# Kernel tuning notes

Measured on AMD Instinct MI355X. Metric: run time of the kernel, lower is better.

The kernel has to match this reference:

```python
import jax, jax.numpy as jnp
import numpy as np

B, N, F, O = 8, 4096, 512, 512
D = F // 8  # fc1/fc2 projection dim = 64


def setup_inputs() -> dict:
    key = jax.random.key(0)
    ks = jax.random.split(key, 8)
    x = jax.random.normal(ks[0], (B, N, F), dtype=jnp.float32)
    mask = jax.random.randint(ks[1], (B, N), 0, 2).astype(jnp.float32)
    s1 = 1.0 / np.sqrt(F)
    w1 = jax.random.uniform(ks[2], (F, D), jnp.float32, -s1, s1)
    b1 = jnp.zeros((D,), jnp.float32)
    w2 = jax.random.uniform(ks[3], (F, D), jnp.float32, -s1, s1)
    b2 = jnp.zeros((D,), jnp.float32)
    s2 = 1.0 / np.sqrt(O)
    weight = jax.random.uniform(ks[4], (F, O), jnp.float32, -s2, s2)
    return {"x": x, "mask": mask, "w1": w1, "b1": b1, "w2": w2, "b2": b2, "weight": weight}


def reference(x, mask, w1, b1, w2, b2, weight):
    # q, k: [B, N, D]
    q = x @ w1 + b1
    k = x @ w2 + b2
    scale = jnp.sqrt(jnp.asarray(D, x.dtype))
    # sim: [B, N, N]
    sim = jnp.einsum('bnd,bmd->bnm', q, k) / scale
    # NOTE: mask.unsqueeze(-1) -> [B, N, 1]: masks QUERY rows (faithful to source)
    neg = jnp.asarray(-1e12, x.dtype)
    sim = sim + (1.0 - mask)[:, :, None] * neg
    adj = jax.nn.softmax(sim, axis=-1) * mask[:, :, None]
    support = x @ weight  # [B, N, O]
    return jnp.einsum('bnm,bmo->bno', adj, support)
```

## Files before the change

kernel.cpp:

```cpp
#include <hip/hip_runtime.h>

constexpr int BB = 8, NN = 4096, FF = 512, DD = 64, OO = 512;

using short8  = __attribute__((ext_vector_type(8))) short;
using ushort8 = __attribute__((ext_vector_type(8))) unsigned short;
using ushort4v= __attribute__((ext_vector_type(4))) unsigned short;
using f32x4   = __attribute__((ext_vector_type(4))) float;

__device__ __forceinline__ unsigned short f2bf(float f) {
  unsigned int u = __builtin_bit_cast(unsigned int, f);
  return (unsigned short)((u + 0x7FFFu + ((u >> 16) & 1u)) >> 16);
}

__device__ __forceinline__ f32x4 mfma16(short8 a, short8 b, f32x4 c) {
  return __builtin_amdgcn_mfma_f32_16x16x32_bf16(a, b, c, 0, 0, 0);
}

__device__ __forceinline__ void gl_lds16(const void* g, void* s) {
  __builtin_amdgcn_global_load_lds(
      (const __attribute__((address_space(1))) unsigned int*)g,
      (__attribute__((address_space(3))) unsigned int*)s,
      16, 0, 0);
}

__global__ void cast_x(const float* __restrict__ x, unsigned short* __restrict__ xb) {
  size_t base = ((size_t)blockIdx.x * 256 + threadIdx.x) * 8;
  float4 a = *(const float4*)(x + base);
  float4 b = *(const float4*)(x + base + 4);
  ushort8 o;
  o[0]=f2bf(a.x); o[1]=f2bf(a.y); o[2]=f2bf(a.z); o[3]=f2bf(a.w);
  o[4]=f2bf(b.x); o[5]=f2bf(b.y); o[6]=f2bf(b.z); o[7]=f2bf(b.w);
  *(ushort8*)(xb + base) = o;
}

__global__ void build_w(const float* __restrict__ w1, const float* __restrict__ w2,
                        const float* __restrict__ wgt,
                        const float* __restrict__ b1, const float* __restrict__ b2,
                        unsigned short* __restrict__ Wt, float* __restrict__ bias) {
  int idx = blockIdx.x * 256 + threadIdx.x;
  int j = idx >> 9, kk = idx & 511;
  float v = (j < 64) ? w1[kk * 64 + j]
          : (j < 128) ? w2[kk * 64 + (j - 64)]
                      : wgt[(size_t)kk * 512 + (j - 128)];
  Wt[(size_t)j * 512 + kk] = f2bf(v);
  if (kk == 0) bias[j] = (j < 64) ? b1[j] : (j < 128) ? b2[j - 64] : 0.f;
}

__global__ void compact_rows(const float* __restrict__ mask, int* __restrict__ cnt,
                             int* __restrict__ ridx) {
  __shared__ int wsum[4];
  __shared__ int base;
  const int b = blockIdx.x;
  const int t = threadIdx.x, lane = t & 63, w = t >> 6;
  if (t == 0) base = 0;
  __syncthreads();
  for (int it = 0; it < 16; ++it) {
    int r = it * 256 + t;
    bool act = mask[(b << 12) + r] != 0.f;
    unsigned long long bal = __ballot(act);
    int pre = __popcll(bal & ((1ull << lane) - 1ull));
    if (lane == 0) wsum[w] = __popcll(bal);
    __syncthreads();
    int woff = 0;
    for (int i = 0; i < w; ++i) woff += wsum[i];
    int tot = wsum[0] + wsum[1] + wsum[2] + wsum[3];
    if (act) ridx[(b << 12) + base + woff + pre] = r;
    __syncthreads();
    if (t == 0) base += tot;
    __syncthreads();
  }
  if (t == 0) cnt[b] = base;
}

__global__ void zero_masked(const float* __restrict__ mask, float* __restrict__ out) {
  int gid = blockIdx.x * 256 + threadIdx.x;
  int r = gid >> 7, c = (gid & 127) * 4;
  if (mask[r] == 0.f) {
    float4 z = {0.f, 0.f, 0.f, 0.f};
    *(float4*)(out + (size_t)r * 512 + c) = z;
  }
}

__global__ __launch_bounds__(256, 2) void proj_gemm(
    const unsigned short* __restrict__ X, const unsigned short* __restrict__ Wt,
    const float* __restrict__ bias,
    unsigned short* __restrict__ QK, unsigned short* __restrict__ SupT) {
  __shared__ __align__(16) unsigned short Abuf[128 * 64];
  __shared__ __align__(16) unsigned short Bbuf[128 * 64];
  const int t = threadIdx.x, lane = t & 63, w = t >> 6;
  const int nblk = blockIdx.x;
  const int m0 = blockIdx.y * 128, n0 = nblk * 128;
  const int wm = w & 1, wn = w >> 1;

  f32x4 acc[4][4] = {};
  for (int kt = 0; kt < 8; ++kt) {
    for (int i = 0; i < 4; ++i) {
      int c = i * 4 + w;
      int row = c * 8 + (lane >> 3);
      int k0 = (lane & 7) * 8;
      gl_lds16(X + (size_t)(m0 + row) * 512 + kt * 64 + k0, &Abuf[c * 512]);
      gl_lds16(Wt + (size_t)(n0 + row) * 512 + kt * 64 + k0, &Bbuf[c * 512]);
    }
    __syncthreads();
    short8 af[4][2], bfr[4][2];
    for (int mi = 0; mi < 4; ++mi)
      for (int kc = 0; kc < 2; ++kc) {
        int row = wm * 64 + mi * 16 + (lane & 15);
        int d = kc * 32 + (lane >> 4) * 8;
        af[mi][kc] = *(const short8*)&Abuf[row * 64 + d];
      }
    for (int ni = 0; ni < 4; ++ni)
      for (int kc = 0; kc < 2; ++kc) {
        int col = wn * 64 + ni * 16 + (lane & 15);
        int d = kc * 32 + (lane >> 4) * 8;
        bfr[ni][kc] = *(const short8*)&Bbuf[col * 64 + d];
      }
    for (int mi = 0; mi < 4; ++mi)
      for (int ni = 0; ni < 4; ++ni)
        for (int kc = 0; kc < 2; ++kc)
          acc[mi][ni] = mfma16(af[mi][kc], bfr[ni][kc], acc[mi][ni]);
    __syncthreads();
  }
  for (int mi = 0; mi < 4; ++mi)
    for (int ni = 0; ni < 4; ++ni) {
      int col_g = n0 + wn * 64 + ni * 16 + (lane & 15);
      int row0 = m0 + wm * 64 + mi * 16 + ((lane >> 4) * 4);
      float bv = bias[col_g];
      if (nblk == 0) {
        for (int j = 0; j < 4; ++j)
          QK[(size_t)(row0 + j) * 128 + col_g] = f2bf(acc[mi][ni][j] + bv);
      } else {
        int scol = col_g - 128;
        int b = row0 >> 12, rl = row0 & 4095;
        ushort4v pk;
        for (int j = 0; j < 4; ++j) pk[j] = f2bf(acc[mi][ni][j] + bv);
        *(ushort4v*)&SupT[(size_t)(b * 512 + scol) * 4096 + rl] = pk;
      }
    }
}

__global__ __launch_bounds__(512, 2) void attn_kernel(
    const unsigned short* __restrict__ QK, const unsigned short* __restrict__ SupT,
    const int* __restrict__ cnt, const int* __restrict__ ridx,
    float* __restrict__ out) {
  __shared__ __align__(16) unsigned short Kb[3][32 * 64];
  __shared__ __align__(16) unsigned short Vt[3][256 * 32];
  __shared__ __align__(16) unsigned short Pb[2][64 * 40];
  __shared__ float lsh[2][64];
  __shared__ int rsh[64];

  const int batch = blockIdx.x & 7;
  const int rest  = blockIdx.x >> 3;
  const int chunk = rest >> 1, colh = rest & 1;
  const int n_act = cnt[batch];
  if (chunk * 64 >= n_act) return;
  const int rem = min(64, n_act - chunk * 64);

  const int t = threadIdx.x, lane = t & 63, w = t >> 6;
  const int keybase = batch << 12;
  const int wm = w >> 2;
  const int wq = w & 3;
  const int fms = wq >> 1, ks = wq & 1;
  const int wo = w & 3;

  if (t < 64) rsh[t] = ridx[(batch << 12) + chunk * 64 + min(t, rem - 1)];
  __syncthreads();

  short8 aq[2];
  {
    int rl = rsh[wm * 32 + fms * 16 + (lane & 15)];
    for (int kc = 0; kc < 2; ++kc)
      aq[kc] = *(const short8*)&QK[(size_t)(keybase + rl) * 128 + kc * 32 + (lane >> 4) * 8];
  }

  f32x4 acc[2][4] = {};
  float lacc[4] = {0.f, 0.f, 0.f, 0.f};

  auto stage = [&](int p, int key0) {
    if (w < 4) {
      int key = w * 8 + (lane >> 3);
      int q = lane & 7;
      int d0 = (q ^ (key & 7)) * 8;
      gl_lds16(QK + (size_t)(keybase + key0 + key) * 128 + 64 + d0, &Kb[p][w * 512]);
    }
    for (int i = 0; i < 2; ++i) {
      int c = i * 8 + w;
      int colL = c * 16 + (lane >> 2);
      int q = lane & 3;
      int k0 = (q ^ ((colL >> 1) & 3)) * 8;
      gl_lds16(SupT + (size_t)(batch * 512 + colh * 256 + colL) * 4096 + key0 + k0,
               &Vt[p][c * 512]);
    }
  };

  stage(0, 0);
  stage(1, 32);
  for (int kt = 0; kt < 128; ++kt) {
    const int p = kt % 3;
    const int pb = kt & 1;
    if (kt < 127) {
      if (w < 4) asm volatile("s_waitcnt vmcnt(3)" ::: "memory");
      else       asm volatile("s_waitcnt vmcnt(2)" ::: "memory");
    } else {
      asm volatile("s_waitcnt vmcnt(0)" ::: "memory");
    }
    asm volatile("s_barrier" ::: "memory");

    if (kt < 126) stage((kt + 2) % 3, (kt + 2) * 32);

    {
      f32x4 sa = {0.f, 0.f, 0.f, 0.f};
      int key = ks * 16 + (lane & 15);
      __builtin_amdgcn_s_setprio(1);
      for (int kc = 0; kc < 2; ++kc) {
        int dblk = kc * 4 + (lane >> 4);
        int blk = dblk ^ (key & 7);
        short8 bk = *(const short8*)&Kb[p][key * 64 + blk * 8];
        sa = mfma16(aq[kc], bk, sa);
      }
      __builtin_amdgcn_s_setprio(0);
      int rl0 = wm * 32 + fms * 16 + (lane >> 4) * 4;
      for (int j = 0; j < 4; ++j) {
        float pv = __expf(sa[j] * 0.125f);
        lacc[j] += pv;
        Pb[pb][(rl0 + j) * 40 + key] = f2bf(pv);
      }
    }
    asm volatile("s_waitcnt lgkmcnt(0)" ::: "memory");
    asm volatile("s_barrier" ::: "memory");

    short8 pa[2];
    for (int fm = 0; fm < 2; ++fm) {
      int row = wm * 32 + fm * 16 + (lane & 15);
      pa[fm] = *(const short8*)&Pb[pb][row * 40 + (lane >> 4) * 8];
    }
    __builtin_amdgcn_s_setprio(1);
    for (int ni = 0; ni < 4; ++ni) {
      int colL = wo * 64 + ni * 16 + (lane & 15);
      int blk = (lane >> 4) ^ ((colL >> 1) & 3);
      short8 vb = *(const short8*)&Vt[p][colL * 32 + blk * 8];
      acc[0][ni] = mfma16(pa[0], vb, acc[0][ni]);
      acc[1][ni] = mfma16(pa[1], vb, acc[1][ni]);
    }
    __builtin_amdgcn_s_setprio(0);
  }

  for (int j = 0; j < 4; ++j) {
    float v = lacc[j];
    v += __shfl_xor(v, 1); v += __shfl_xor(v, 2);
    v += __shfl_xor(v, 4); v += __shfl_xor(v, 8);
    lacc[j] = v;
  }
  if ((lane & 15) == 0) {
    int rl0 = wm * 32 + fms * 16 + (lane >> 4) * 4;
    for (int j = 0; j < 4; ++j) lsh[ks][rl0 + j] = lacc[j];
  }
  __syncthreads();

  for (int fm = 0; fm < 2; ++fm)
    for (int ni = 0; ni < 4; ++ni) {
      int colL = wo * 64 + ni * 16 + (lane & 15);
      int sl0 = wm * 32 + fm * 16 + (lane >> 4) * 4;
      for (int j = 0; j < 4; ++j) {
        if (sl0 + j < rem) {
          float linv = 1.f / (lsh[0][sl0 + j] + lsh[1][sl0 + j]);
          int rl = rsh[sl0 + j];
          out[(size_t)(keybase + rl) * 512 + colh * 256 + colL] = acc[fm][ni][j] * linv;
        }
      }
    }
}

extern "C" void kernel_launch(void* const* d_in, const int* in_sizes, int n_in,
                              void* d_out, int out_size, void* d_ws, size_t ws_size,
                              hipStream_t stream) {
  const float* x    = (const float*)d_in[0];
  const float* mask = (const float*)d_in[1];
  const float* w1   = (const float*)d_in[2];
  const float* b1   = (const float*)d_in[3];
  const float* w2   = (const float*)d_in[4];
  const float* b2   = (const float*)d_in[5];
  const float* wgt  = (const float*)d_in[6];
  float* out = (float*)d_out;

  char* ws = (char*)d_ws;
  unsigned short* Xb   = (unsigned short*)(ws);
  unsigned short* QK   = (unsigned short*)(ws + 33554432);
  unsigned short* SupT = (unsigned short*)(ws + 41943040);
  unsigned short* Wt   = (unsigned short*)(ws + 75497472);
  float* bias          = (float*)(ws + 76152832);
  int*   cnt           = (int*)(ws + 76417536);
  int*   ridx          = (int*)(ws + 76417664);

  build_w<<<dim3(1280), dim3(256), 0, stream>>>(w1, w2, wgt, b1, b2, Wt, bias);
  compact_rows<<<dim3(8), dim3(256), 0, stream>>>(mask, cnt, ridx);
  cast_x<<<dim3(8192), dim3(256), 0, stream>>>(x, Xb);
  proj_gemm<<<dim3(5, 256), dim3(256), 0, stream>>>(Xb, Wt, bias, QK, SupT);
  attn_kernel<<<dim3(1024), dim3(512), 0, stream>>>(QK, SupT, cnt, ridx, out);
  zero_masked<<<dim3(16384), dim3(256), 0, stream>>>(mask, out);
}
```

Baseline: 279.7 us.

## Load K and V fragments directly from global into registers, drop LDS staging

The attention kernel no longer stages K and V tiles through a triple-buffered LDS ring filled by global_load_lds. Each wave now loads its own MFMA operand fragments straight from global memory into registers and prefetches the next tile one iteration ahead, removing the per-tile vmcnt wait and one barrier. Occupancy is raised to 4 blocks per CU because the LDS footprint shrinks. The trade is that K fragments are read redundantly across waves, and V fragments are read redundantly across the two wm wave groups, using global and L2 bandwidth in place of LDS sharing, with only one tile of load latency hidden.

```diff
diff --git a/kernel.cpp b/kernel.cpp
--- a/kernel.cpp
+++ b/kernel.cpp
@@ -139,12 +139,10 @@
     }
 }
 
-__global__ __launch_bounds__(512, 2) void attn_kernel(
+__global__ __launch_bounds__(512, 4) void attn_kernel(
     const unsigned short* __restrict__ QK, const unsigned short* __restrict__ SupT,
     const int* __restrict__ cnt, const int* __restrict__ ridx,
     float* __restrict__ out) {
-  __shared__ __align__(16) unsigned short Kb[3][32 * 64];
-  __shared__ __align__(16) unsigned short Vt[3][256 * 32];
   __shared__ __align__(16) unsigned short Pb[2][64 * 40];
   __shared__ float lsh[2][64];
   __shared__ int rsh[64];
@@ -173,76 +171,68 @@
       aq[kc] = *(const short8*)&QK[(size_t)(keybase + rl) * 128 + kc * 32 + (lane >> 4) * 8];
   }
 
+  const unsigned short* Kp =
+      QK + (size_t)(keybase + ks * 16 + (lane & 15)) * 128 + 64 + (lane >> 4) * 8;
+  const unsigned short* Vp =
+      SupT + (size_t)(batch * 512 + colh * 256 + wo * 64 + (lane & 15)) * 4096 + (lane >> 4) * 8;
+
   f32x4 acc[2][4] = {};
   float lacc[4] = {0.f, 0.f, 0.f, 0.f};
 
-  auto stage = [&](int p, int key0) {
-    if (w < 4) {
-      int key = w * 8 + (lane >> 3);
-      int q = lane & 7;
-      int d0 = (q ^ (key & 7)) * 8;
-      gl_lds16(QK + (size_t)(keybase + key0 + key) * 128 + 64 + d0, &Kb[p][w * 512]);
-    }
-    for (int i = 0; i < 2; ++i) {
-      int c = i * 8 + w;
-      int colL = c * 16 + (lane >> 2);
-      int q = lane & 3;
-      int k0 = (q ^ ((colL >> 1) & 3)) * 8;
-      gl_lds16(SupT + (size_t)(batch * 512 + colh * 256 + colL) * 4096 + key0 + k0,
-               &Vt[p][c * 512]);
-    }
-  };
-
-  stage(0, 0);
-  stage(1, 32);
+  short8 kf0 = *(const short8*)(Kp);
+  short8 kf1 = *(const short8*)(Kp + 32);
+  short8 vf0 = *(const short8*)(Vp);
+  short8 vf1 = *(const short8*)(Vp + (size_t)16 * 4096);
+  short8 vf2 = *(const short8*)(Vp + (size_t)32 * 4096);
+  short8 vf3 = *(const short8*)(Vp + (size_t)48 * 4096);
+
+  const int rl0 = wm * 32 + fms * 16 + (lane >> 4) * 4;
+  const int key = ks * 16 + (lane & 15);
+  const int prow = wm * 32 + (lane & 15);
+  const int pcol = (lane >> 4) * 8;
+
   for (int kt = 0; kt < 128; ++kt) {
-    const int p = kt % 3;
     const int pb = kt & 1;
-    if (kt < 127) {
-      if (w < 4) asm volatile("s_waitcnt vmcnt(3)" ::: "memory");
-      else       asm volatile("s_waitcnt vmcnt(2)" ::: "memory");
-    } else {
-      asm volatile("s_waitcnt vmcnt(0)" ::: "memory");
-    }
-    asm volatile("s_barrier" ::: "memory");
-
-    if (kt < 126) stage((kt + 2) % 3, (kt + 2) * 32);
+    f32x4 sa = {0.f, 0.f, 0.f, 0.f};
+    __builtin_amdgcn_s_setprio(1);
+    sa = mfma16(aq[0], kf0, sa);
+    sa = mfma16(aq[1], kf1, sa);
+    __builtin_amdgcn_s_setprio(0);
 
     {
-      f32x4 sa = {0.f, 0.f, 0.f, 0.f};
-      int key = ks * 16 + (lane & 15);
-      __builtin_amdgcn_s_setprio(1);
-      for (int kc = 0; kc < 2; ++kc) {
-        int dblk = kc * 4 + (lane >> 4);
-        int blk = dblk ^ (key & 7);
-        short8 bk = *(const short8*)&Kb[p][key * 64 + blk * 8];
-        sa = mfma16(aq[kc], bk, sa);
-      }
-      __builtin_amdgcn_s_setprio(0);
-      int rl0 = wm * 32 + fms * 16 + (lane >> 4) * 4;
-      for (int j = 0; j < 4; ++j) {
-        float pv = __expf(sa[j] * 0.125f);
-        lacc[j] += pv;
-        Pb[pb][(rl0 + j) * 40 + key] = f2bf(pv);
-      }
+      size_t knext = (kt < 127) ? (size_t)(kt + 1) * 32 : 0;
+      kf0 = *(const short8*)(Kp + knext * 128);
+      kf1 = *(const short8*)(Kp + knext * 128 + 32);
+    }
+
+    for (int j = 0; j < 4; ++j) {
+      float pv = __expf(sa[j] * 0.125f);
+      lacc[j] += pv;
+      Pb[pb][(rl0 + j) * 40 + key] = f2bf(pv);
     }
     asm volatile("s_waitcnt lgkmcnt(0)" ::: "memory");
     asm volatile("s_barrier" ::: "memory");
 
-    short8 pa[2];
-    for (int fm = 0; fm < 2; ++fm) {
-      int row = wm * 32 + fm * 16 + (lane & 15);
-      pa[fm] = *(const short8*)&Pb[pb][row * 40 + (lane >> 4) * 8];
-    }
+    short8 pa0 = *(const short8*)&Pb[pb][prow * 40 + pcol];
+    short8 pa1 = *(const short8*)&Pb[pb][(prow + 16) * 40 + pcol];
     __builtin_amdgcn_s_setprio(1);
-    for (int ni = 0; ni < 4; ++ni) {
-      int colL = wo * 64 + ni * 16 + (lane & 15);
-      int blk = (lane >> 4) ^ ((colL >> 1) & 3);
-      short8 vb = *(const short8*)&Vt[p][colL * 32 + blk * 8];
-      acc[0][ni] = mfma16(pa[0], vb, acc[0][ni]);
-      acc[1][ni] = mfma16(pa[1], vb, acc[1][ni]);
-    }
+    acc[0][0] = mfma16(pa0, vf0, acc[0][0]);
+    acc[1][0] = mfma16(pa1, vf0, acc[1][0]);
+    acc[0][1] = mfma16(pa0, vf1, acc[0][1]);
+    acc[1][1] = mfma16(pa1, vf1, acc[1][1]);
+    acc[0][2] = mfma16(pa0, vf2, acc[0][2]);
+    acc[1][2] = mfma16(pa1, vf2, acc[1][2]);
+    acc[0][3] = mfma16(pa0, vf3, acc[0][3]);
+    acc[1][3] = mfma16(pa1, vf3, acc[1][3]);
     __builtin_amdgcn_s_setprio(0);
+
+    {
+      size_t knext = (kt < 127) ? (size_t)(kt + 1) * 32 : 0;
+      vf0 = *(const short8*)(Vp + knext);
+      vf1 = *(const short8*)(Vp + (size_t)16 * 4096 + knext);
+      vf2 = *(const short8*)(Vp + (size_t)32 * 4096 + knext);
+      vf3 = *(const short8*)(Vp + (size_t)48 * 4096 + knext);
+    }
   }
 
   for (int j = 0; j < 4; ++j) {
@@ -252,7 +242,6 @@
     lacc[j] = v;
   }
   if ((lane & 15) == 0) {
-    int rl0 = wm * 32 + fms * 16 + (lane >> 4) * 4;
     for (int j = 0; j < 4; ++j) lsh[ks][rl0 + j] = lacc[j];
   }
   __syncthreads();
@@ -265,7 +254,8 @@
         if (sl0 + j < rem) {
           float linv = 1.f / (lsh[0][sl0 + j] + lsh[1][sl0 + j]);
           int rl = rsh[sl0 + j];
-          out[(size_t)(keybase + rl) * 512 + colh * 256 + colL] = acc[fm][ni][j] * linv;
+          float av = (fm == 0) ? ((float*)&acc[0][ni])[j] : ((float*)&acc[1][ni])[j];
+          out[(size_t)(keybase + rl) * 512 + colh * 256 + colL] = av * linv;
         }
       }
     }
```

Result: slower. 590.1 us (+111.0%).
